# Performance work log

Hardware: AMD Instinct MI355X
Metric: run time of the kernel (lower is better)

## Reference

```python
import jax, jax.numpy as jnp
import numpy as np

N = 50000      # nodes
E = 800000     # edges (avg degree 16)
F_IN = 128
HID = 128
C = 40
EPS = 1e-5     # BatchNorm1d eps


def setup_inputs() -> dict:
    key = jax.random.key(0)
    ks = jax.random.split(key, 8)

    def glorot(k, shape):
        lim = np.sqrt(6.0 / (shape[0] + shape[1])).astype(np.float32)
        return jax.random.uniform(k, shape, jnp.float32, -lim, lim)

    inp = {
        "features": jax.random.normal(ks[0], (N, F_IN), jnp.float32),
        "edge_index": jax.random.randint(ks[1], (2, E), 0, N, jnp.int32),
        "W1": glorot(ks[2], (F_IN, HID)), "b1": jnp.zeros((HID,), jnp.float32),
        "gamma1": jnp.ones((HID,), jnp.float32), "beta1": jnp.zeros((HID,), jnp.float32),
        "W2": glorot(ks[3], (HID, HID)), "b2": jnp.zeros((HID,), jnp.float32),
        "gamma2": jnp.ones((HID,), jnp.float32), "beta2": jnp.zeros((HID,), jnp.float32),
        "W3": glorot(ks[4], (HID, C)), "b3": jnp.zeros((C,), jnp.float32),
    }
    return inp


def _gcn_norm(edge_index):
    # Add self-loops and compute symmetric normalization D^-1/2 (A+I) D^-1/2
    loops = jnp.arange(N, dtype=edge_index.dtype)
    src = jnp.concatenate([edge_index[0], loops])
    dst = jnp.concatenate([edge_index[1], loops])
    deg = jax.ops.segment_sum(jnp.ones((E + N,), jnp.float32), dst, num_segments=N)
    dinv = jax.lax.rsqrt(jnp.maximum(deg, 1.0))
    return src, dst, dinv[src] * dinv[dst]  # per-edge norm coefficient


def _gcn_conv(x, W, b, src, dst, norm):
    h = x @ W                                   # [N, out]
    msg = h[src] * norm[:, None]                # gather + scale, [E+N, out]
    return jax.ops.segment_sum(msg, dst, num_segments=N) + b


def _bn(x, gamma, beta):
    # training-mode BatchNorm1d over the node axis (biased variance)
    mu = jnp.mean(x, axis=0)
    var = jnp.mean(jnp.square(x - mu), axis=0)
    return (x - mu) * jax.lax.rsqrt(var + EPS) * gamma + beta


def reference(features, edge_index, W1, b1, gamma1, beta1, W2, b2, gamma2, beta2, W3, b3):
    src, dst, norm = _gcn_norm(edge_index)
    h = jax.nn.relu(_bn(_gcn_conv(features, W1, b1, src, dst, norm), gamma1, beta1))
    h = jax.nn.relu(_bn(_gcn_conv(h, W2, b2, src, dst, norm), gamma2, beta2))
    h = _gcn_conv(h, W3, b3, src, dst, norm)
    return jax.nn.log_softmax(h, axis=-1)
```

## Files before the change

kernel.cpp:

```cpp
#include <hip/hip_runtime.h>
#include <math.h>

#define FEAT 128
#define NCLS 40
#define BN_EPS 1e-5f
#define CAP 64

typedef unsigned short u16;
typedef unsigned int u32;
typedef __attribute__((ext_vector_type(8))) short bf16x8;
typedef __attribute__((ext_vector_type(4))) float f32x4;

__device__ inline u32 f2b2(float a, float b) {
    u32 ua = __float_as_uint(a), ub = __float_as_uint(b);
    ua = (ua + 0x7fffu + ((ua >> 16) & 1u)) >> 16;
    ub = (ub + 0x7fffu + ((ub >> 16) & 1u)) >> 16;
    return ua | (ub << 16);
}
__device__ inline u16 f2b1(float a) {
    u32 ua = __float_as_uint(a);
    return (u16)((ua + 0x7fffu + ((ua >> 16) & 1u)) >> 16);
}
__device__ inline float b2f(u16 u) { return __uint_as_float((u32)u << 16); }
__device__ inline float blo(u32 u) { return __uint_as_float(u << 16); }
__device__ inline float bhi(u32 u) { return __uint_as_float(u & 0xffff0000u); }

__device__ inline void b8acc(uint4 u, float w, float* a) {
    a[0] = fmaf(w, blo(u.x), a[0]); a[1] = fmaf(w, bhi(u.x), a[1]);
    a[2] = fmaf(w, blo(u.y), a[2]); a[3] = fmaf(w, bhi(u.y), a[3]);
    a[4] = fmaf(w, blo(u.z), a[4]); a[5] = fmaf(w, bhi(u.z), a[5]);
    a[6] = fmaf(w, blo(u.w), a[6]); a[7] = fmaf(w, bhi(u.w), a[7]);
}


__device__ inline void stage_wt(const float* __restrict__ W, u16* Wt) {
    const float4* W4 = (const float4*)W;
#pragma unroll
    for (int i = 0; i < 16; ++i) {
        int li = threadIdx.x + i * 256;
        int k = li >> 5;
        int n0 = (li & 31) * 4;
        int s = k >> 5, quad = (k >> 3) & 3, koff = k & 7;
        int nt = n0 >> 4, nl0 = n0 & 15;
        int base = ((s * 8 + nt) * 64 + quad * 16) * 8 + koff;
        float4 w = W4[li];
        Wt[base + (nl0 + 0) * 8] = f2b1(w.x);
        Wt[base + (nl0 + 1) * 8] = f2b1(w.y);
        Wt[base + (nl0 + 2) * 8] = f2b1(w.z);
        Wt[base + (nl0 + 3) * 8] = f2b1(w.w);
    }
}

__device__ inline void stage_wt40(const float* __restrict__ W, u16* Wt) {
    for (int e = threadIdx.x; e < 12 * 64 * 8; e += 256) {
        int j = e & 7;
        int lane = (e >> 3) & 63;
        int tile = e >> 9;
        int s = tile / 3, nt = tile % 3;
        int n = nt * 16 + (lane & 15);
        int k = s * 32 + (lane >> 4) * 8 + j;
        float v = (n < NCLS) ? W[k * NCLS + n] : 0.f;
        Wt[e] = f2b1(v);
    }
}

__global__ __launch_bounds__(256) void k_init(
    const float* __restrict__ W1, const float* __restrict__ W2,
    const float* __restrict__ W3, u16* __restrict__ Wg,
    uint4* __restrict__ zbase, int zcount, int zblocks,
    const int* __restrict__ edges, u16* __restrict__ ew, int twoE)
{
    int b = blockIdx.x;
    if (b == 0) stage_wt(W1, Wg);
    else if (b == 1) stage_wt(W2, Wg + 128 * 128);
    else if (b == 2) stage_wt40(W3, Wg + 2 * 128 * 128);
    else if (b < 3 + zblocks) {
        int idx = (b - 3) * 256 + threadIdx.x;
        if (idx < zcount) zbase[idx] = make_uint4(0, 0, 0, 0);
    } else {
        int idx = ((b - 3 - zblocks) * 256 + threadIdx.x) * 8;
        if (idx + 8 <= twoE) {
            int4 a = *(const int4*)(edges + idx);
            int4 c = *(const int4*)(edges + idx + 4);
            uint4 o;
            o.x = (u32)(a.x & 0xffff) | ((u32)a.y << 16);
            o.y = (u32)(a.z & 0xffff) | ((u32)a.w << 16);
            o.z = (u32)(c.x & 0xffff) | ((u32)c.y << 16);
            o.w = (u32)(c.z & 0xffff) | ((u32)c.w << 16);
            *(uint4*)(ew + idx) = o;
        } else {
            for (int e = idx; e < twoE; ++e) ew[e] = (u16)edges[e];
        }
    }
}

__device__ inline void mfma_core(const uint4* __restrict__ wt4, const bf16x8* bfrag,
                                 u16* __restrict__ Y, int node, int M, int nl, int quad) {
    int lane = quad * 16 + nl;
    f32x4 acc[8];
#pragma unroll
    for (int nt = 0; nt < 8; ++nt) acc[nt] = (f32x4){0.f, 0.f, 0.f, 0.f};
#pragma unroll
    for (int s = 0; s < 4; ++s) {
#pragma unroll
        for (int nt = 0; nt < 8; ++nt) {
            uint4 aw = wt4[(s * 8 + nt) * 64 + lane];
            bf16x8 af = *(bf16x8*)&aw;
            acc[nt] = __builtin_amdgcn_mfma_f32_16x16x32_bf16(af, bfrag[s], acc[nt], 0, 0, 0);
        }
    }
    if (node < M) {
#pragma unroll
        for (int nt = 0; nt < 8; ++nt) {
            uint2 o;
            o.x = f2b2(acc[nt][0], acc[nt][1]);
            o.y = f2b2(acc[nt][2], acc[nt][3]);
            *(uint2*)&Y[(size_t)node * 128 + nt * 16 + quad * 4] = o;
        }
    }
}


__global__ __launch_bounds__(256, 8) void k_l1_fill(
    const float* __restrict__ X, const u16* __restrict__ Wg, u16* __restrict__ Y, int M,
    const u16* __restrict__ srcw, const u16* __restrict__ dstw,
    int* __restrict__ cnt, u16* __restrict__ col, int E,
    int gemmBlocks, int nchunks)
{
    if ((int)blockIdx.x < gemmBlocks) {
        int wv = threadIdx.x >> 6;
        int lane = threadIdx.x & 63;
        int nl = lane & 15, quad = lane >> 4;
        int node = blockIdx.x * 64 + wv * 16 + nl;

        bf16x8 bfrag[4];
        if (node < M) {
            const float4* xr = (const float4*)(X + (size_t)node * 128);
#pragma unroll
            for (int s = 0; s < 4; ++s) {
                float4 xa = xr[s * 8 + quad * 2];
                float4 xb = xr[s * 8 + quad * 2 + 1];
                uint4 bu;
                bu.x = f2b2(xa.x, xa.y); bu.y = f2b2(xa.z, xa.w);
                bu.z = f2b2(xb.x, xb.y); bu.w = f2b2(xb.z, xb.w);
                bfrag[s] = *(bf16x8*)&bu;
            }
        } else {
            uint4 z = make_uint4(0, 0, 0, 0);
#pragma unroll
            for (int s = 0; s < 4; ++s) bfrag[s] = *(bf16x8*)&z;
        }
        mfma_core((const uint4*)Wg, bfrag, Y, node, M, nl, quad);
    } else {
        int fb = blockIdx.x - gemmBlocks;
        int part = fb & 7;
        int chunk = fb >> 3;
        int lo = (int)(((long long)M * part) >> 3);
        int hi = (int)(((long long)M * (part + 1)) >> 3);
        int per = ((E + nchunks - 1) / nchunks + 7) & ~7;
        int e0 = chunk * per;
        int e1 = e0 + per; if (e1 > E) e1 = E;

        for (int eb = e0 + (int)threadIdx.x * 8; eb < e1; eb += 2048) {
            if (eb + 8 <= e1) {
                uint4 du = *(const uint4*)(dstw + eb);
                uint4 su = *(const uint4*)(srcw + eb);
                int dd[8] = {(int)(du.x & 0xffffu), (int)(du.x >> 16),
                             (int)(du.y & 0xffffu), (int)(du.y >> 16),
                             (int)(du.z & 0xffffu), (int)(du.z >> 16),
                             (int)(du.w & 0xffffu), (int)(du.w >> 16)};
                u16 ss[8] = {(u16)(su.x & 0xffffu), (u16)(su.x >> 16),
                             (u16)(su.y & 0xffffu), (u16)(su.y >> 16),
                             (u16)(su.z & 0xffffu), (u16)(su.z >> 16),
                             (u16)(su.w & 0xffffu), (u16)(su.w >> 16)};
#pragma unroll
                for (int k = 0; k < 8; ++k) {
                    int d = dd[k];
                    if (d >= lo && d < hi) {
                        int c = atomicAdd(&cnt[d], 1);
                        if (c < CAP) col[(size_t)d * CAP + c] = ss[k];
                    }
                }
            } else {
                for (int e = eb; e < e1; ++e) {
                    int d = (int)dstw[e];
                    if (d >= lo && d < hi) {
                        int c = atomicAdd(&cnt[d], 1);
                        if (c < CAP) col[(size_t)d * CAP + c] = srcw[e];
                    }
                }
            }
        }
    }
}


__device__ inline void build_bfrag_bn(const u16* __restrict__ X, int node, int M,
                                      int quad, const float* scs, const float* shs,
                                      bf16x8* bfrag) {
    if (node < M) {
        const uint4* xr = (const uint4*)(X + (size_t)node * 128);
#pragma unroll
        for (int s = 0; s < 4; ++s) {
            int k0 = s * 32 + quad * 8;
            uint4 xu = xr[s * 4 + quad];
            float4 sc0 = *(const float4*)&scs[k0];
            float4 sc1 = *(const float4*)&scs[k0 + 4];
            float4 sh0 = *(const float4*)&shs[k0];
            float4 sh1 = *(const float4*)&shs[k0 + 4];
            float v0 = fmaxf(fmaf(blo(xu.x), sc0.x, sh0.x), 0.f);
            float v1 = fmaxf(fmaf(bhi(xu.x), sc0.y, sh0.y), 0.f);
            float v2 = fmaxf(fmaf(blo(xu.y), sc0.z, sh0.z), 0.f);
            float v3 = fmaxf(fmaf(bhi(xu.y), sc0.w, sh0.w), 0.f);
            float v4 = fmaxf(fmaf(blo(xu.z), sc1.x, sh1.x), 0.f);
            float v5 = fmaxf(fmaf(bhi(xu.z), sc1.y, sh1.y), 0.f);
            float v6 = fmaxf(fmaf(blo(xu.w), sc1.z, sh1.z), 0.f);
            float v7 = fmaxf(fmaf(bhi(xu.w), sc1.w, sh1.w), 0.f);
            uint4 bu;
            bu.x = f2b2(v0, v1); bu.y = f2b2(v2, v3);
            bu.z = f2b2(v4, v5); bu.w = f2b2(v6, v7);
            bfrag[s] = *(bf16x8*)&bu;
        }
    } else {
        uint4 z = make_uint4(0, 0, 0, 0);
#pragma unroll
        for (int s = 0; s < 4; ++s) bfrag[s] = *(bf16x8*)&z;
    }
}

__global__ __launch_bounds__(256, 2) void k_mfma_l2(
    const u16* __restrict__ X, const u16* __restrict__ Wg,
    const float* __restrict__ sums, const float* __restrict__ gamma,
    const float* __restrict__ beta, u16* __restrict__ Y, int M)
{
    __shared__ __align__(16) u16 Wt[128 * 128];
    __shared__ __align__(16) float scs[128], shs[128];

    if (threadIdx.x < 128) {
        int f = threadIdx.x;
        float inv_n = 1.f / (float)M;
        float mu = sums[f] * inv_n;
        float var = sums[128 + f] * inv_n - mu * mu;
        float rs = rsqrtf(var + BN_EPS);
        float sc = gamma[f] * rs;
        scs[f] = sc;
        shs[f] = beta[f] - mu * sc;
    }
    {
        uint4* d4 = (uint4*)Wt;
        const uint4* s4 = (const uint4*)Wg;
#pragma unroll
        for (int i = 0; i < 8; ++i) d4[threadIdx.x + i * 256] = s4[threadIdx.x + i * 256];
    }
    __syncthreads();

    int wv = threadIdx.x >> 6;
    int lane = threadIdx.x & 63;
    int nl = lane & 15, quad = lane >> 4;
    int nodeA = blockIdx.x * 128 + wv * 16 + nl;
    int nodeB = nodeA + 64;

    bf16x8 bfragA[4], bfragB[4];
    build_bfrag_bn(X, nodeA, M, quad, scs, shs, bfragA);
    build_bfrag_bn(X, nodeB, M, quad, scs, shs, bfragB);

    const uint4* wt4 = (const uint4*)Wt;
    f32x4 accA[8], accB[8];
#pragma unroll
    for (int nt = 0; nt < 8; ++nt) {
        accA[nt] = (f32x4){0.f, 0.f, 0.f, 0.f};
        accB[nt] = (f32x4){0.f, 0.f, 0.f, 0.f};
    }
#pragma unroll
    for (int s = 0; s < 4; ++s) {
#pragma unroll
        for (int nt = 0; nt < 8; ++nt) {
            uint4 aw = wt4[(s * 8 + nt) * 64 + lane];
            bf16x8 af = *(bf16x8*)&aw;
            accA[nt] = __builtin_amdgcn_mfma_f32_16x16x32_bf16(af, bfragA[s], accA[nt], 0, 0, 0);
            accB[nt] = __builtin_amdgcn_mfma_f32_16x16x32_bf16(af, bfragB[s], accB[nt], 0, 0, 0);
        }
    }
    if (nodeA < M) {
#pragma unroll
        for (int nt = 0; nt < 8; ++nt) {
            uint2 o;
            o.x = f2b2(accA[nt][0], accA[nt][1]);
            o.y = f2b2(accA[nt][2], accA[nt][3]);
            *(uint2*)&Y[(size_t)nodeA * 128 + nt * 16 + quad * 4] = o;
        }
    }
    if (nodeB < M) {
#pragma unroll
        for (int nt = 0; nt < 8; ++nt) {
            uint2 o;
            o.x = f2b2(accB[nt][0], accB[nt][1]);
            o.y = f2b2(accB[nt][2], accB[nt][3]);
            *(uint2*)&Y[(size_t)nodeB * 128 + nt * 16 + quad * 4] = o;
        }
    }
}


__global__ __launch_bounds__(256) void k_mfma_l3(
    const u16* __restrict__ X, const u16* __restrict__ Wg,
    const float* __restrict__ sums, const float* __restrict__ gamma,
    const float* __restrict__ beta, u16* __restrict__ Y, int M)
{
    __shared__ __align__(16) u16 Wt[12 * 64 * 8];
    __shared__ __align__(16) float scs[128], shs[128];

    if (threadIdx.x < 128) {
        int f = threadIdx.x;
        float inv_n = 1.f / (float)M;
        float mu = sums[f] * inv_n;
        float var = sums[128 + f] * inv_n - mu * mu;
        float rs = rsqrtf(var + BN_EPS);
        float sc = gamma[f] * rs;
        scs[f] = sc;
        shs[f] = beta[f] - mu * sc;
    }
    {
        uint4* d4 = (uint4*)Wt;
        const uint4* s4 = (const uint4*)Wg;
#pragma unroll
        for (int i = 0; i < 3; ++i) d4[threadIdx.x + i * 256] = s4[threadIdx.x + i * 256];
    }
    __syncthreads();

    int wv = threadIdx.x >> 6;
    int lane = threadIdx.x & 63;
    int nl = lane & 15, quad = lane >> 4;
    int node = blockIdx.x * 64 + wv * 16 + nl;

    bf16x8 bfrag[4];
    build_bfrag_bn(X, node, M, quad, scs, shs, bfrag);

    const uint4* wt4 = (const uint4*)Wt;
    f32x4 acc[3];
#pragma unroll
    for (int nt = 0; nt < 3; ++nt) acc[nt] = (f32x4){0.f, 0.f, 0.f, 0.f};
#pragma unroll
    for (int s = 0; s < 4; ++s) {
#pragma unroll
        for (int nt = 0; nt < 3; ++nt) {
            uint4 aw = wt4[(s * 3 + nt) * 64 + lane];
            bf16x8 af = *(bf16x8*)&aw;
            acc[nt] = __builtin_amdgcn_mfma_f32_16x16x32_bf16(af, bfrag[s], acc[nt], 0, 0, 0);
        }
    }
    if (node < M) {
#pragma unroll
        for (int nt = 0; nt < 3; ++nt) {
            int c0 = nt * 16 + quad * 4;
            if (c0 < NCLS) {
                uint2 o;
                o.x = f2b2(acc[nt][0], acc[nt][1]);
                o.y = f2b2(acc[nt][2], acc[nt][3]);
                *(uint2*)&Y[(size_t)node * NCLS + c0] = o;
            }
        }
    }
}


__global__ __launch_bounds__(256) void k_agg128_bn(
    const u16* __restrict__ t, const int* __restrict__ cnt,
    const u16* __restrict__ col, const float* __restrict__ bias,
    u16* __restrict__ out, float* __restrict__ sums, int n)
{
    int wid = threadIdx.x >> 4;
    int lane = threadIdx.x & 15;
    float4 bA = ((const float4*)bias)[lane * 2];
    float4 bB = ((const float4*)bias)[lane * 2 + 1];

    float bs[8], bq[8];
#pragma unroll
    for (int k = 0; k < 8; ++k) { bs[k] = 0.f; bq[k] = 0.f; }

    for (int i0 = blockIdx.x * 16; i0 < n; i0 += gridDim.x * 16) {
        int i = i0 + wid;
        if (i < n) {
            int c = cnt[i];
            int deg = c < CAP ? c : CAP;
            int beg = i * CAP, end = beg + deg;
            float di = rsqrtf((float)(c + 1));

            float a[8];
            {
                uint4 su = ((const uint4*)(t + (size_t)i * 128))[lane];
                a[0] = di * blo(su.x); a[1] = di * bhi(su.x);
                a[2] = di * blo(su.y); a[3] = di * bhi(su.y);
                a[4] = di * blo(su.z); a[5] = di * bhi(su.z);
                a[6] = di * blo(su.w); a[7] = di * bhi(su.w);
            }

            for (int j = beg; j < end; j += 8) {
                uint4 c0 = *(const uint4*)(col + j);
                int sr[8] = {
                    (int)(c0.x & 0xffffu), (int)(c0.x >> 16),
                    (int)(c0.y & 0xffffu), (int)(c0.y >> 16),
                    (int)(c0.z & 0xffffu), (int)(c0.z >> 16),
                    (int)(c0.w & 0xffffu), (int)(c0.w >> 16)};
                float w[8]; uint4 v[8];
                if (j + 8 <= end) {
#pragma unroll
                    for (int k = 0; k < 8; ++k) {
                        int sck = cnt[sr[k]];
                        v[k] = ((const uint4*)(t + (size_t)sr[k] * 128))[lane];
                        w[k] = rsqrtf((float)(sck + 1));
                    }
                } else {
#pragma unroll
                    for (int k = 0; k < 8; ++k) {
                        bool valid = (j + k) < end;
                        int s = valid ? sr[k] : 0;
                        int sck = cnt[s];
                        v[k] = ((const uint4*)(t + (size_t)s * 128))[lane];
                        w[k] = valid ? rsqrtf((float)(sck + 1)) : 0.f;
                    }
                }
#pragma unroll
                for (int k = 0; k < 8; ++k) b8acc(v[k], w[k], a);
            }

            float vv[8];
            vv[0] = fmaf(di, a[0], bA.x); vv[1] = fmaf(di, a[1], bA.y);
            vv[2] = fmaf(di, a[2], bA.z); vv[3] = fmaf(di, a[3], bA.w);
            vv[4] = fmaf(di, a[4], bB.x); vv[5] = fmaf(di, a[5], bB.y);
            vv[6] = fmaf(di, a[6], bB.z); vv[7] = fmaf(di, a[7], bB.w);
            uint4 o;
            o.x = f2b2(vv[0], vv[1]); o.y = f2b2(vv[2], vv[3]);
            o.z = f2b2(vv[4], vv[5]); o.w = f2b2(vv[6], vv[7]);
            ((uint4*)(out + (size_t)i * 128))[lane] = o;
#pragma unroll
            for (int k = 0; k < 8; ++k) {
                bs[k] += vv[k];
                bq[k] = fmaf(vv[k], vv[k], bq[k]);
            }
        }
    }

    __shared__ float red[16][128];
#pragma unroll
    for (int k = 0; k < 8; ++k) red[wid][lane * 8 + k] = bs[k];
    __syncthreads();
    if (threadIdx.x < 128) {
        float v = 0.f;
#pragma unroll
        for (int w = 0; w < 16; ++w) v += red[w][threadIdx.x];
        atomicAdd(&sums[threadIdx.x], v);
    }
    __syncthreads();
#pragma unroll
    for (int k = 0; k < 8; ++k) red[wid][lane * 8 + k] = bq[k];
    __syncthreads();
    if (threadIdx.x < 128) {
        float v = 0.f;
#pragma unroll
        for (int w = 0; w < 16; ++w) v += red[w][threadIdx.x];
        atomicAdd(&sums[128 + threadIdx.x], v);
    }
}


__global__ __launch_bounds__(256) void k_agg40(
    const u16* __restrict__ t, const int* __restrict__ cnt,
    const u16* __restrict__ col, const float* __restrict__ bias,
    float* __restrict__ out, int n)
{
    int i = blockIdx.x * 32 + (threadIdx.x >> 3);
    if (i >= n) return;
    int l = threadIdx.x & 7;
    bool act = l < 5;
    int c = cnt[i];
    int deg = c < CAP ? c : CAP;
    int beg = i * CAP, end = beg + deg;
    float di = rsqrtf((float)(c + 1));

    float a[8] = {0.f, 0.f, 0.f, 0.f, 0.f, 0.f, 0.f, 0.f};
    if (act) {
        uint4 su = ((const uint4*)(t + (size_t)i * NCLS))[l];
        a[0] = di * blo(su.x); a[1] = di * bhi(su.x);
        a[2] = di * blo(su.y); a[3] = di * bhi(su.y);
        a[4] = di * blo(su.z); a[5] = di * bhi(su.z);
        a[6] = di * blo(su.w); a[7] = di * bhi(su.w);
    }
    for (int j = beg; j < end; j += 8) {
        uint4 c0 = *(const uint4*)(col + j);
        int sr[8] = {
            (int)(c0.x & 0xffffu), (int)(c0.x >> 16),
            (int)(c0.y & 0xffffu), (int)(c0.y >> 16),
            (int)(c0.z & 0xffffu), (int)(c0.z >> 16),
            (int)(c0.w & 0xffffu), (int)(c0.w >> 16)};
        float w[8]; uint4 v[8];
        if (j + 8 <= end) {
#pragma unroll
            for (int k = 0; k < 8; ++k) {
                int sck = cnt[sr[k]];
                v[k] = act ? ((const uint4*)(t + (size_t)sr[k] * NCLS))[l]
                           : make_uint4(0, 0, 0, 0);
                w[k] = rsqrtf((float)(sck + 1));
            }
        } else {
#pragma unroll
            for (int k = 0; k < 8; ++k) {
                bool valid = (j + k) < end;
                int s = valid ? sr[k] : 0;
                int sck = cnt[s];
                v[k] = act ? ((const uint4*)(t + (size_t)s * NCLS))[l]
                           : make_uint4(0, 0, 0, 0);
                w[k] = valid ? rsqrtf((float)(sck + 1)) : 0.f;
            }
        }
#pragma unroll
        for (int k = 0; k < 8; ++k) b8acc(v[k], w[k], a);
    }

    float v[8];
    float m = -INFINITY;
    if (act) {
        float4 b0 = *(const float4*)(bias + l * 8);
        float4 b1 = *(const float4*)(bias + l * 8 + 4);
        v[0] = fmaf(di, a[0], b0.x); v[1] = fmaf(di, a[1], b0.y);
        v[2] = fmaf(di, a[2], b0.z); v[3] = fmaf(di, a[3], b0.w);
        v[4] = fmaf(di, a[4], b1.x); v[5] = fmaf(di, a[5], b1.y);
        v[6] = fmaf(di, a[6], b1.z); v[7] = fmaf(di, a[7], b1.w);
#pragma unroll
        for (int k = 0; k < 8; ++k) m = fmaxf(m, v[k]);
    }
#pragma unroll
    for (int d = 1; d < 8; d <<= 1) m = fmaxf(m, __shfl_xor(m, d, 8));
    float es = 0.f;
    if (act) {
#pragma unroll
        for (int k = 0; k < 8; ++k) es += expf(v[k] - m);
    }
#pragma unroll
    for (int d = 1; d < 8; d <<= 1) es += __shfl_xor(es, d, 8);
    float ls = logf(es);
    if (act) {
        float4 o0, o1;
        o0.x = v[0] - m - ls; o0.y = v[1] - m - ls;
        o0.z = v[2] - m - ls; o0.w = v[3] - m - ls;
        o1.x = v[4] - m - ls; o1.y = v[5] - m - ls;
        o1.z = v[6] - m - ls; o1.w = v[7] - m - ls;
        *(float4*)(out + (size_t)i * NCLS + l * 8) = o0;
        *(float4*)(out + (size_t)i * NCLS + l * 8 + 4) = o1;
    }
}


extern "C" void kernel_launch(void* const* d_in, const int* in_sizes, int n_in,
                              void* d_out, int out_size, void* d_ws, size_t ws_size,
                              hipStream_t stream) {
    const float* features = (const float*)d_in[0];
    const int* edge_index = (const int*)d_in[1];
    const float* W1 = (const float*)d_in[2];
    const float* b1 = (const float*)d_in[3];
    const float* gamma1 = (const float*)d_in[4];
    const float* beta1 = (const float*)d_in[5];
    const float* W2 = (const float*)d_in[6];
    const float* b2 = (const float*)d_in[7];
    const float* gamma2 = (const float*)d_in[8];
    const float* beta2 = (const float*)d_in[9];
    const float* W3 = (const float*)d_in[10];
    const float* b3 = (const float*)d_in[11];
    float* out = (float*)d_out;

    int n = in_sizes[0] / FEAT;
    int E = in_sizes[1] / 2;

    char* p = (char*)d_ws;
    auto alloc = [&](size_t bytes) -> void* {
        void* r = (void*)p;
        p += (bytes + 255) & ~(size_t)255;
        return r;
    };
    int* cnt     = (int*)alloc((size_t)n * 4);
    float* sums  = (float*)alloc(512 * 4);
    size_t zspan = (size_t)((char*)(sums + 512) - (char*)cnt);
    u16* colb    = (u16*)alloc((size_t)n * CAP * 2 + 64);
    u16* hb      = (u16*)alloc((size_t)n * 128 * 2);
    u16* ab      = (u16*)alloc((size_t)n * 128 * 2);
    u16* wgb     = (u16*)alloc((size_t)(2 * 128 * 128 + 12 * 64 * 8) * 2);
    u16* ew      = (u16*)alloc((size_t)2 * E * 2);

    float* sums1 = sums;
    float* sums2 = sums + 256;
    u16* Wg1 = wgb;
    u16* Wg2 = wgb + 128 * 128;
    u16* Wg3 = wgb + 2 * 128 * 128;
    u16* srcw = ew;
    u16* dstw = ew + E;

    int gb64 = (n + 63) / 64;
    int gb128 = (n + 127) / 128;
    int gb16 = (n + 15) / 16;
    int gb32 = (n + 31) / 32;
    int aggGrid = gb16 < 1024 ? gb16 : 1024;

    int zcount = (int)(zspan / 16);
    int zblocks = (zcount + 255) / 256;
    int twoE = 2 * E;
    int cblocks = (twoE / 8 + 255) / 256;
    k_init<<<3 + zblocks + cblocks, 256, 0, stream>>>(W1, W2, W3, wgb,
                                                      (uint4*)cnt, zcount, zblocks,
                                                      edge_index, ew, twoE);

    int nchunks = 160;
    k_l1_fill<<<gb64 + nchunks * 8, 256, 0, stream>>>(features, Wg1, hb, n,
                                                      srcw, dstw, cnt, colb, E,
                                                      gb64, nchunks);

    k_agg128_bn<<<aggGrid, 256, 0, stream>>>(hb, cnt, colb, b1, ab, sums1, n);

    k_mfma_l2<<<gb128, 256, 0, stream>>>(ab, Wg2, sums1, gamma1, beta1, hb, n);
    k_agg128_bn<<<aggGrid, 256, 0, stream>>>(hb, cnt, colb, b2, ab, sums2, n);

    k_mfma_l3<<<gb64, 256, 0, stream>>>(ab, Wg3, sums2, gamma2, beta2, hb, n);
    k_agg40<<<gb32, 256, 0, stream>>>(hb, cnt, colb, b3, out, n);
}
```

Before: 302.0 us.

## Pre-bucket edges by destination range and cache neighbor degrees in packed column list

```diff
diff --git a/kernel.cpp b/kernel.cpp
--- a/kernel.cpp
+++ b/kernel.cpp
@@ -67,30 +67,64 @@
 __global__ __launch_bounds__(256) void k_init(
     const float* __restrict__ W1, const float* __restrict__ W2,
     const float* __restrict__ W3, u16* __restrict__ Wg,
-    uint4* __restrict__ zbase, int zcount, int zblocks,
-    const int* __restrict__ edges, u16* __restrict__ ew, int twoE)
+    const int* __restrict__ edges, u32* __restrict__ ebuf,
+    int* __restrict__ bucketCnt, int E, int bcap, float inv8n)
 {
     int b = blockIdx.x;
     if (b == 0) stage_wt(W1, Wg);
     else if (b == 1) stage_wt(W2, Wg + 128 * 128);
     else if (b == 2) stage_wt40(W3, Wg + 2 * 128 * 128);
-    else if (b < 3 + zblocks) {
-        int idx = (b - 3) * 256 + threadIdx.x;
-        if (idx < zcount) zbase[idx] = make_uint4(0, 0, 0, 0);
-    } else {
-        int idx = ((b - 3 - zblocks) * 256 + threadIdx.x) * 8;
-        if (idx + 8 <= twoE) {
-            int4 a = *(const int4*)(edges + idx);
-            int4 c = *(const int4*)(edges + idx + 4);
-            uint4 o;
-            o.x = (u32)(a.x & 0xffff) | ((u32)a.y << 16);
-            o.y = (u32)(a.z & 0xffff) | ((u32)a.w << 16);
-            o.z = (u32)(c.x & 0xffff) | ((u32)c.y << 16);
-            o.w = (u32)(c.z & 0xffff) | ((u32)c.w << 16);
-            *(uint4*)(ew + idx) = o;
+    else {
+        __shared__ int hcnt[8];
+        __shared__ int hbase[8];
+        int t = threadIdx.x;
+        if (t < 8) hcnt[t] = 0;
+        __syncthreads();
+
+        int e0 = (b - 3) * 2048 + t * 8;
+        u32 pk[8]; int bk[8];
+        int nval = 0;
+        if (e0 + 8 <= E) {
+            int4 s0 = *(const int4*)(edges + e0);
+            int4 s1 = *(const int4*)(edges + e0 + 4);
+            int4 d0 = *(const int4*)(edges + E + e0);
+            int4 d1 = *(const int4*)(edges + E + e0 + 4);
+            int ss[8] = {s0.x, s0.y, s0.z, s0.w, s1.x, s1.y, s1.z, s1.w};
+            int dd[8] = {d0.x, d0.y, d0.z, d0.w, d1.x, d1.y, d1.z, d1.w};
+#pragma unroll
+            for (int k = 0; k < 8; ++k) {
+                pk[k] = (u32)ss[k] | ((u32)dd[k] << 16);
+                int bx = (int)((float)dd[k] * inv8n);
+                bk[k] = bx > 7 ? 7 : bx;
+            }
+            nval = 8;
         } else {
-            for (int e = idx; e < twoE; ++e) ew[e] = (u16)edges[e];
-        }
+#pragma unroll
+            for (int k = 0; k < 8; ++k) {
+                int e = e0 + k;
+                if (e < E) {
+                    int s = edges[e], d = edges[E + e];
+                    pk[k] = (u32)s | ((u32)d << 16);
+                    int bx = (int)((float)d * inv8n);
+                    bk[k] = bx > 7 ? 7 : bx;
+                    nval = k + 1;
+                }
+            }
+        }
+#pragma unroll
+        for (int k = 0; k < 8; ++k)
+            if (k < nval) atomicAdd(&hcnt[bk[k]], 1);
+        __syncthreads();
+        if (t < 8) hbase[t] = hcnt[t] ? atomicAdd(&bucketCnt[t], hcnt[t]) : 0;
+        __syncthreads();
+        if (t < 8) hcnt[t] = 0;
+        __syncthreads();
+#pragma unroll
+        for (int k = 0; k < 8; ++k)
+            if (k < nval) {
+                int off = atomicAdd(&hcnt[bk[k]], 1);
+                ebuf[(size_t)bk[k] * bcap + hbase[bk[k]] + off] = pk[k];
+            }
     }
 }
 
@@ -123,9 +157,9 @@
 
 __global__ __launch_bounds__(256, 8) void k_l1_fill(
     const float* __restrict__ X, const u16* __restrict__ Wg, u16* __restrict__ Y, int M,
-    const u16* __restrict__ srcw, const u16* __restrict__ dstw,
-    int* __restrict__ cnt, u16* __restrict__ col, int E,
-    int gemmBlocks, int nchunks)
+    const u32* __restrict__ ebuf, const int* __restrict__ bucketCnt, int bcap,
+    int* __restrict__ cnt, u16* __restrict__ col,
+    int gemmBlocks, int C)
 {
     if ((int)blockIdx.x < gemmBlocks) {
         int wv = threadIdx.x >> 6;
@@ -155,39 +189,27 @@
         int fb = blockIdx.x - gemmBlocks;
         int part = fb & 7;
         int chunk = fb >> 3;
-        int lo = (int)(((long long)M * part) >> 3);
-        int hi = (int)(((long long)M * (part + 1)) >> 3);
-        int per = ((E + nchunks - 1) / nchunks + 7) & ~7;
-        int e0 = chunk * per;
-        int e1 = e0 + per; if (e1 > E) e1 = E;
-
-        for (int eb = e0 + (int)threadIdx.x * 8; eb < e1; eb += 2048) {
-            if (eb + 8 <= e1) {
-                uint4 du = *(const uint4*)(dstw + eb);
-                uint4 su = *(const uint4*)(srcw + eb);
-                int dd[8] = {(int)(du.x & 0xffffu), (int)(du.x >> 16),
-                             (int)(du.y & 0xffffu), (int)(du.y >> 16),
-                             (int)(du.z & 0xffffu), (int)(du.z >> 16),
-                             (int)(du.w & 0xffffu), (int)(du.w >> 16)};
-                u16 ss[8] = {(u16)(su.x & 0xffffu), (u16)(su.x >> 16),
-                             (u16)(su.y & 0xffffu), (u16)(su.y >> 16),
-                             (u16)(su.z & 0xffffu), (u16)(su.z >> 16),
-                             (u16)(su.w & 0xffffu), (u16)(su.w >> 16)};
+        int bcnt = bucketCnt[part];
+        const u32* be = ebuf + (size_t)part * bcap;
+        int step = C << 11;
+
+        for (int e = (chunk << 11) + (int)threadIdx.x * 8; e < bcnt; e += step) {
+            if (e + 8 <= bcnt) {
+                uint4 p0 = *(const uint4*)(be + e);
+                uint4 p1 = *(const uint4*)(be + e + 4);
+                u32 pk[8] = {p0.x, p0.y, p0.z, p0.w, p1.x, p1.y, p1.z, p1.w};
 #pragma unroll
                 for (int k = 0; k < 8; ++k) {
-                    int d = dd[k];
-                    if (d >= lo && d < hi) {
-                        int c = atomicAdd(&cnt[d], 1);
-                        if (c < CAP) col[(size_t)d * CAP + c] = ss[k];
-                    }
+                    int d = (int)(pk[k] >> 16);
+                    int c = atomicAdd(&cnt[d], 1);
+                    if (c < CAP) col[(size_t)d * CAP + c] = (u16)(pk[k] & 0xffffu);
                 }
             } else {
-                for (int e = eb; e < e1; ++e) {
-                    int d = (int)dstw[e];
-                    if (d >= lo && d < hi) {
-                        int c = atomicAdd(&cnt[d], 1);
-                        if (c < CAP) col[(size_t)d * CAP + c] = srcw[e];
-                    }
+                for (int q = e; q < bcnt; ++q) {
+                    u32 p = be[q];
+                    int d = (int)(p >> 16);
+                    int c = atomicAdd(&cnt[d], 1);
+                    if (c < CAP) col[(size_t)d * CAP + c] = (u16)(p & 0xffffu);
                 }
             }
         }
@@ -364,9 +386,11 @@
 }
 
 
+template<bool FIRST>
 __global__ __launch_bounds__(256) void k_agg128_bn(
     const u16* __restrict__ t, const int* __restrict__ cnt,
-    const u16* __restrict__ col, const float* __restrict__ bias,
+    const u16* __restrict__ col, u32* __restrict__ colw,
+    const float* __restrict__ bias,
     u16* __restrict__ out, float* __restrict__ sums, int n)
 {
     int wid = threadIdx.x >> 4;
@@ -395,33 +419,67 @@
                 a[6] = di * blo(su.w); a[7] = di * bhi(su.w);
             }
 
-            for (int j = beg; j < end; j += 8) {
-                uint4 c0 = *(const uint4*)(col + j);
-                int sr[8] = {
-                    (int)(c0.x & 0xffffu), (int)(c0.x >> 16),
-                    (int)(c0.y & 0xffffu), (int)(c0.y >> 16),
-                    (int)(c0.z & 0xffffu), (int)(c0.z >> 16),
-                    (int)(c0.w & 0xffffu), (int)(c0.w >> 16)};
-                float w[8]; uint4 v[8];
-                if (j + 8 <= end) {
+            if (FIRST) {
+                for (int j = beg; j < end; j += 8) {
+                    uint4 c0 = *(const uint4*)(col + j);
+                    int sr[8] = {
+                        (int)(c0.x & 0xffffu), (int)(c0.x >> 16),
+                        (int)(c0.y & 0xffffu), (int)(c0.y >> 16),
+                        (int)(c0.z & 0xffffu), (int)(c0.z >> 16),
+                        (int)(c0.w & 0xffffu), (int)(c0.w >> 16)};
+                    float w[8]; uint4 v[8]; int su[8]; int sck[8];
+                    if (j + 8 <= end) {
+#pragma unroll
+                        for (int k = 0; k < 8; ++k) {
+                            su[k] = sr[k];
+                            sck[k] = cnt[su[k]];
+                            v[k] = ((const uint4*)(t + (size_t)su[k] * 128))[lane];
+                            w[k] = rsqrtf((float)(sck[k] + 1));
+                        }
+                    } else {
+#pragma unroll
+                        for (int k = 0; k < 8; ++k) {
+                            bool valid = (j + k) < end;
+                            su[k] = valid ? sr[k] : 0;
+                            sck[k] = cnt[su[k]];
+                            v[k] = ((const uint4*)(t + (size_t)su[k] * 128))[lane];
+                            w[k] = valid ? rsqrtf((float)(sck[k] + 1)) : 0.f;
+                        }
+                    }
+                    if (lane == 0) {
+                        uint4 o;
+                        o.x = (u32)su[0] | ((u32)sck[0] << 16);
+                        o.y = (u32)su[1] | ((u32)sck[1] << 16);
+                        o.z = (u32)su[2] | ((u32)sck[2] << 16);
+                        o.w = (u32)su[3] | ((u32)sck[3] << 16);
+                        *(uint4*)(colw + j) = o;
+                    } else if (lane == 1) {
+                        uint4 o;
+                        o.x = (u32)su[4] | ((u32)sck[4] << 16);
+                        o.y = (u32)su[5] | ((u32)sck[5] << 16);
+                        o.z = (u32)su[6] | ((u32)sck[6] << 16);
+                        o.w = (u32)su[7] | ((u32)sck[7] << 16);
+                        *(uint4*)(colw + j + 4) = o;
+                    }
+#pragma unroll
+                    for (int k = 0; k < 8; ++k) b8acc(v[k], w[k], a);
+                }
+            } else {
+                for (int j = beg; j < end; j += 8) {
+                    uint4 p0 = *(const uint4*)(colw + j);
+                    uint4 p1 = *(const uint4*)(colw + j + 4);
+                    u32 pk[8] = {p0.x, p0.y, p0.z, p0.w, p1.x, p1.y, p1.z, p1.w};
+                    float w[8]; uint4 v[8];
 #pragma unroll
                     for (int k = 0; k < 8; ++k) {
-                        int sck = cnt[sr[k]];
-                        v[k] = ((const uint4*)(t + (size_t)sr[k] * 128))[lane];
-                        w[k] = rsqrtf((float)(sck + 1));
+                        int s = (int)(pk[k] & 0xffffu);
+                        float w0 = rsqrtf((float)(pk[k] >> 16) + 1.f);
+                        v[k] = ((const uint4*)(t + (size_t)s * 128))[lane];
+                        w[k] = ((j + k) < end) ? w0 : 0.f;
                     }
-                } else {
-#pragma unroll
-                    for (int k = 0; k < 8; ++k) {
-                        bool valid = (j + k) < end;
-                        int s = valid ? sr[k] : 0;
-                        int sck = cnt[s];
-                        v[k] = ((const uint4*)(t + (size_t)s * 128))[lane];
-                        w[k] = valid ? rsqrtf((float)(sck + 1)) : 0.f;
-                    }
+#pragma unroll
+                    for (int k = 0; k < 8; ++k) b8acc(v[k], w[k], a);
                 }
-#pragma unroll
-                for (int k = 0; k < 8; ++k) b8acc(v[k], w[k], a);
             }
 
             float vv[8];
@@ -466,7 +524,7 @@
 
 __global__ __launch_bounds__(256) void k_agg40(
     const u16* __restrict__ t, const int* __restrict__ cnt,
-    const u16* __restrict__ col, const float* __restrict__ bias,
+    const u32* __restrict__ colw, const float* __restrict__ bias,
     float* __restrict__ out, int n)
 {
     int i = blockIdx.x * 32 + (threadIdx.x >> 3);
@@ -487,34 +545,17 @@
         a[6] = di * blo(su.w); a[7] = di * bhi(su.w);
     }
     for (int j = beg; j < end; j += 8) {
-        uint4 c0 = *(const uint4*)(col + j);
-        int sr[8] = {
-            (int)(c0.x & 0xffffu), (int)(c0.x >> 16),
-            (int)(c0.y & 0xffffu), (int)(c0.y >> 16),
-            (int)(c0.z & 0xffffu), (int)(c0.z >> 16),
-            (int)(c0.w & 0xffffu), (int)(c0.w >> 16)};
-        float w[8]; uint4 v[8];
-        if (j + 8 <= end) {
-#pragma unroll
-            for (int k = 0; k < 8; ++k) {
-                int sck = cnt[sr[k]];
-                v[k] = act ? ((const uint4*)(t + (size_t)sr[k] * NCLS))[l]
-                           : make_uint4(0, 0, 0, 0);
-                w[k] = rsqrtf((float)(sck + 1));
-            }
-        } else {
-#pragma unroll
-            for (int k = 0; k < 8; ++k) {
-                bool valid = (j + k) < end;
-                int s = valid ? sr[k] : 0;
-                int sck = cnt[s];
-                v[k] = act ? ((const uint4*)(t + (size_t)s * NCLS))[l]
-                           : make_uint4(0, 0, 0, 0);
-                w[k] = valid ? rsqrtf((float)(sck + 1)) : 0.f;
-            }
-        }
-#pragma unroll
-        for (int k = 0; k < 8; ++k) b8acc(v[k], w[k], a);
+        uint4 p0 = *(const uint4*)(colw + j);
+        uint4 p1 = *(const uint4*)(colw + j + 4);
+        u32 pk[8] = {p0.x, p0.y, p0.z, p0.w, p1.x, p1.y, p1.z, p1.w};
+#pragma unroll
+        for (int k = 0; k < 8; ++k) {
+            int s = (int)(pk[k] & 0xffffu);
+            float w0 = rsqrtf((float)(pk[k] >> 16) + 1.f);
+            uint4 v = act ? ((const uint4*)(t + (size_t)s * NCLS))[l]
+                          : make_uint4(0, 0, 0, 0);
+            b8acc(v, ((j + k) < end) ? w0 : 0.f, a);
+        }
     }
 
     float v[8];
@@ -577,47 +618,47 @@
         p += (bytes + 255) & ~(size_t)255;
         return r;
     };
-    int* cnt     = (int*)alloc((size_t)n * 4);
-    float* sums  = (float*)alloc(512 * 4);
-    size_t zspan = (size_t)((char*)(sums + 512) - (char*)cnt);
-    u16* colb    = (u16*)alloc((size_t)n * CAP * 2 + 64);
-    u16* hb      = (u16*)alloc((size_t)n * 128 * 2);
-    u16* ab      = (u16*)alloc((size_t)n * 128 * 2);
-    u16* wgb     = (u16*)alloc((size_t)(2 * 128 * 128 + 12 * 64 * 8) * 2);
-    u16* ew      = (u16*)alloc((size_t)2 * E * 2);
+    int* cnt       = (int*)alloc((size_t)n * 4);
+    float* sums    = (float*)alloc(512 * 4);
+    int* bucketCnt = (int*)alloc(8 * 4);
+    size_t zspan   = (size_t)((char*)(bucketCnt + 8) - (char*)cnt);
+    u16* colb      = (u16*)alloc((size_t)n * CAP * 2 + 64);
+    u32* colw      = (u32*)alloc((size_t)n * CAP * 4 + 64);
+    u16* hb        = (u16*)alloc((size_t)n * 128 * 2);
+    u16* ab        = (u16*)alloc((size_t)n * 128 * 2);
+    u16* wgb       = (u16*)alloc((size_t)(2 * 128 * 128 + 12 * 64 * 8) * 2);
+    int bcap       = E / 8 + 16384;
+    u32* ebuf      = (u32*)alloc((size_t)8 * bcap * 4);
 
     float* sums1 = sums;
     float* sums2 = sums + 256;
     u16* Wg1 = wgb;
     u16* Wg2 = wgb + 128 * 128;
     u16* Wg3 = wgb + 2 * 128 * 128;
-    u16* srcw = ew;
-    u16* dstw = ew + E;
 
     int gb64 = (n + 63) / 64;
     int gb128 = (n + 127) / 128;
     int gb16 = (n + 15) / 16;
     int gb32 = (n + 31) / 32;
     int aggGrid = gb16 < 1024 ? gb16 : 1024;
-
-    int zcount = (int)(zspan / 16);
-    int zblocks = (zcount + 255) / 256;
-    int twoE = 2 * E;
-    int cblocks = (twoE / 8 + 255) / 256;
-    k_init<<<3 + zblocks + cblocks, 256, 0, stream>>>(W1, W2, W3, wgb,
-                                                      (uint4*)cnt, zcount, zblocks,
-                                                      edge_index, ew, twoE);
-
-    int nchunks = 160;
-    k_l1_fill<<<gb64 + nchunks * 8, 256, 0, stream>>>(features, Wg1, hb, n,
-                                                      srcw, dstw, cnt, colb, E,
-                                                      gb64, nchunks);
-
-    k_agg128_bn<<<aggGrid, 256, 0, stream>>>(hb, cnt, colb, b1, ab, sums1, n);
+    float inv8n = 8.0f / (float)n;
+
+    hipMemsetAsync(cnt, 0, zspan, stream);
+
+    int nbb = (E + 2047) / 2048;
+    k_init<<<3 + nbb, 256, 0, stream>>>(W1, W2, W3, wgb,
+                                        edge_index, ebuf, bucketCnt, E, bcap, inv8n);
+
+    int C = 64;
+    k_l1_fill<<<gb64 + C * 8, 256, 0, stream>>>(features, Wg1, hb, n,
+                                                ebuf, bucketCnt, bcap,
+                                                cnt, colb, gb64, C);
+
+    k_agg128_bn<true><<<aggGrid, 256, 0, stream>>>(hb, cnt, colb, colw, b1, ab, sums1, n);
 
     k_mfma_l2<<<gb128, 256, 0, stream>>>(ab, Wg2, sums1, gamma1, beta1, hb, n);
-    k_agg128_bn<<<aggGrid, 256, 0, stream>>>(hb, cnt, colb, b2, ab, sums2, n);
+    k_agg128_bn<false><<<aggGrid, 256, 0, stream>>>(hb, cnt, colb, colw, b2, ab, sums2, n);
 
     k_mfma_l3<<<gb64, 256, 0, stream>>>(ab, Wg3, sums2, gamma2, beta2, hb, n);
-    k_agg40<<<gb32, 256, 0, stream>>>(hb, cnt, colb, b3, out, n);
-}
+    k_agg40<<<gb32, 256, 0, stream>>>(hb, cnt, colw, b3, out, n);
+}
```

After: 296.8 us. About the same (-1.7%).
